# Kernel optimization log

Hardware: AMD Instinct MI355X
Metric: run time of the kernel (lower is better)

Reference implementation:

```python
import jax, jax.numpy as jnp
import numpy as np

EPS = 1e-12


def qsplit(x):
    # [..., 4n] with block layout [r|i|j|k] -> [..., n, 4]
    s = x.shape
    n = s[-1] // 4
    return jnp.swapaxes(x.reshape(s[:-1] + (4, n)), -1, -2)


def qmerge(q):
    # [..., n, 4] -> [..., 4n] block layout (transpose(-1,-2).view in torch)
    s = q.shape
    return jnp.swapaxes(q, -1, -2).reshape(s[:-2] + (s[-2] * 4,))


def qnormalize(q):
    # F.normalize(p=2, dim=-1)
    n = jnp.linalg.norm(q, axis=-1, keepdims=True)
    return q / jnp.maximum(n, EPS)


def qmul(q, r):
    # Hamilton product, last axis = (w, x, y, z)
    qw, qx, qy, qz = q[..., 0], q[..., 1], q[..., 2], q[..., 3]
    rw, rx, ry, rz = r[..., 0], r[..., 1], r[..., 2], r[..., 3]
    return jnp.stack([
        qw * rw - qx * rx - qy * ry - qz * rz,
        qw * rx + qx * rw + qy * rz - qz * ry,
        qw * ry - qx * rz + qy * rw + qz * rx,
        qw * rz + qx * ry - qy * rx + qz * rw,
    ], axis=-1)


def qlinear(x, W, b=None):
    # quaternion linear: x [..., 4*n_in], W [4, n_in, n_out]
    xr, xi, xj, xk = jnp.split(x, 4, axis=-1)
    Wr, Wi, Wj, Wk = W[0], W[1], W[2], W[3]
    out = jnp.concatenate([
        xr @ Wr - xi @ Wi - xj @ Wj - xk @ Wk,
        xr @ Wi + xi @ Wr + xj @ Wk - xk @ Wj,
        xr @ Wj - xi @ Wk + xj @ Wr + xk @ Wi,
        xr @ Wk + xi @ Wj - xj @ Wi + xk @ Wr,
    ], axis=-1)
    return out if b is None else out + b


def setup_inputs() -> dict:
    key = jax.random.key(0)
    ks = jax.random.split(key, 7)
    T_enc, T_tgt, B, D, H = 100, 26, 512, 96, 1024
    d4, h4 = D // 4, H // 4
    inp = jax.random.normal(ks[0], (T_enc, B, D), dtype=jnp.float32)
    target = jax.random.normal(ks[1], (T_tgt, B, D), dtype=jnp.float32)
    Wx = jax.random.normal(ks[2], (4, d4, h4), dtype=jnp.float32) * 0.05
    bx = jnp.zeros((H,), dtype=jnp.float32)
    Wh = jax.random.normal(ks[3], (4, h4, h4), dtype=jnp.float32) * 0.05
    Wl = jax.random.normal(ks[4], (4, h4, d4), dtype=jnp.float32) * 0.05
    bl = jnp.zeros((D,), dtype=jnp.float32)
    return {"inp": inp, "target": target, "Wx": Wx, "bx": bx, "Wh": Wh, "Wl": Wl, "bl": bl}


def reference(inp, target, Wx, bx, Wh, Wl, bl):
    B = inp.shape[1]
    H = Wh.shape[1] * 4

    def rnn_step(h, xt):
        h_new = jnp.tanh(qlinear(xt, Wx, bx) + qlinear(h, Wh))
        return h_new, h_new

    def predict(hseq, pre):
        # quaternion linear + per-quaternion L2 normalize + residual Hamilton product
        pred = qlinear(hseq, Wl, bl)
        qn = qnormalize(qsplit(pred))
        return qmerge(qmul(qn, qsplit(pre)))

    h0 = jnp.zeros((B, H), dtype=inp.dtype)
    h_last, hs = jax.lax.scan(rnn_step, h0, inp)  # hs: [T_enc, B, H]
    out_enc = predict(hs, inp)

    def dec_step(carry, _):
        h, x = carry
        h_new = jnp.tanh(qlinear(x, Wx, bx) + qlinear(h, Wh))
        pred = predict(h_new, x)
        return (h_new, pred), pred

    T_dec = target.shape[0] - 1
    _, out_dec = jax.lax.scan(dec_step, (h_last, target[0]), None, length=T_dec)
    return out_enc, out_dec
```

## Files before the change

### kernel.cpp

```cpp
#include <hip/hip_runtime.h>
#include <cstdint>

#define TENC 100
#define TDEC 25
#define BATCH 512
#define DIN 96
#define HDIM 1024

__device__ __constant__ int q_widx[4][4] = {{0,1,2,3},{1,0,3,2},{2,3,0,1},{3,2,1,0}};
__device__ __constant__ float q_sgn[4][4] = {{1.f,-1.f,-1.f,-1.f},
                                             {1.f, 1.f, 1.f,-1.f},
                                             {1.f,-1.f, 1.f, 1.f},
                                             {1.f, 1.f,-1.f, 1.f}};

__global__ void build_eff_kernel(const float* __restrict__ W, float* __restrict__ M,
                                 int nin, int nout) {
    int idx = blockIdx.x * blockDim.x + threadIdx.x;
    int ncol = nout * 4;
    int total = nin * 4 * ncol;
    if (idx >= total) return;
    int col = idx % ncol;
    int k = idx / ncol;
    int c = k / nin, m = k - c * nin;
    int comp = col / nout, o = col - comp * nout;
    M[idx] = q_sgn[comp][c] * W[(size_t)(q_widx[comp][c] * nin + m) * nout + o];
}

__device__ inline float xla_tanh(float x) {
    float ax = fabsf(x);
    if (ax < 0.0004f) return x;
    float t = fminf(fmaxf(x, -7.99881172180175781f), 7.99881172180175781f);
    float x2 = __fmul_rn(t, t);
    float p = -2.76076847742355e-16f;
    p = __fadd_rn(__fmul_rn(p, x2), 2.00018790482477e-13f);
    p = __fadd_rn(__fmul_rn(p, x2), -8.60467152213735e-11f);
    p = __fadd_rn(__fmul_rn(p, x2), 5.12229709037114e-08f);
    p = __fadd_rn(__fmul_rn(p, x2), 1.48572235717979e-05f);
    p = __fadd_rn(__fmul_rn(p, x2), 6.37261928875436e-04f);
    p = __fadd_rn(__fmul_rn(p, x2), 4.89352455891786e-03f);
    float num = __fmul_rn(t, p);
    float q = 1.19825839466702e-06f;
    q = __fadd_rn(__fmul_rn(q, x2), 1.18534705686654e-04f);
    q = __fadd_rn(__fmul_rn(q, x2), 2.26843463243900e-03f);
    q = __fadd_rn(__fmul_rn(q, x2), 4.89352518554385e-03f);
    return __fdiv_rn(num, q);
}

__global__ __launch_bounds__(256)
void rnn_part(const float* __restrict__ X,
              const float* __restrict__ Hin,
              const float* __restrict__ Mx,
              const float* __restrict__ Mh,
              float* __restrict__ parts) {
    __shared__ __align__(16) float As[2][64][68];
    __shared__ __align__(16) float Bs[2][64][64];
    __shared__ __align__(16) float Xs[24][68];
    __shared__ __align__(16) float Ms[24][64];

    const int tid = threadIdx.x;
    const int tx = tid & 15, ty = tid >> 4;
    const int c0 = blockIdx.x * 64;
    const int r0 = blockIdx.y * 64;
    const int z  = blockIdx.z;
    const int lk = tid & 63, lr = tid >> 6;
    const size_t SH = (size_t)BATCH * HDIM;

    float areg[16], breg[16];

    {
        const int k0 = z * 256;
        #pragma unroll
        for (int i = 0; i < 16; ++i)
            areg[i] = Hin[(size_t)(r0 + lr + 4 * i) * 1024 + k0 + lk];
        #pragma unroll
        for (int i = 0; i < 16; ++i)
            breg[i] = Mh[(size_t)(k0 + lr + 4 * i) * 1024 + c0 + lk];
    }
    #pragma unroll
    for (int i = 0; i < 6; ++i) {
        int idx = tid + 256 * i;
        int row = idx / 24, kk = idx - row * 24;
        Xs[kk][row] = X[(size_t)(r0 + row) * 96 + z * 24 + kk];
    }
    #pragma unroll
    for (int i = 0; i < 6; ++i) {
        int idx = tid + 256 * i;
        int kk = idx >> 6, col = idx & 63;
        Ms[kk][col] = Mx[(size_t)(z * 24 + kk) * 1024 + c0 + col];
    }
    #pragma unroll
    for (int i = 0; i < 16; ++i) As[0][lk][lr + 4 * i] = areg[i];
    #pragma unroll
    for (int i = 0; i < 16; ++i) Bs[0][lr + 4 * i][lk] = breg[i];
    __syncthreads();

    {
        float xa[4][4];
        #pragma unroll
        for (int i = 0; i < 4; ++i)
            #pragma unroll
            for (int j = 0; j < 4; ++j) xa[i][j] = 0.f;
        #pragma unroll 4
        for (int kk = 0; kk < 24; ++kk) {
            float4 av = *reinterpret_cast<const float4*>(&Xs[kk][ty * 4]);
            float4 bv = *reinterpret_cast<const float4*>(&Ms[kk][tx * 4]);
            float aa[4] = {av.x, av.y, av.z, av.w};
            float bb[4] = {bv.x, bv.y, bv.z, bv.w};
            #pragma unroll
            for (int i = 0; i < 4; ++i)
                #pragma unroll
                for (int j = 0; j < 4; ++j)
                    xa[i][j] = __fadd_rn(xa[i][j], __fmul_rn(aa[i], bb[j]));
        }
        float* pp = parts + (size_t)(4 + z) * SH;
        const int ccol = c0 + tx * 4;
        #pragma unroll
        for (int i = 0; i < 4; ++i)
            *reinterpret_cast<float4*>(pp + (size_t)(r0 + ty * 4 + i) * 1024 + ccol) =
                make_float4(xa[i][0], xa[i][1], xa[i][2], xa[i][3]);
    }

    float acc[4][4];
    #pragma unroll
    for (int i = 0; i < 4; ++i)
        #pragma unroll
        for (int j = 0; j < 4; ++j) acc[i][j] = 0.f;

    for (int kb = 0; kb < 4; ++kb) {
        const int cur = kb & 1;
        if (kb < 3) {
            const int k0 = z * 256 + (kb + 1) * 64;
            #pragma unroll
            for (int i = 0; i < 16; ++i)
                areg[i] = Hin[(size_t)(r0 + lr + 4 * i) * 1024 + k0 + lk];
            #pragma unroll
            for (int i = 0; i < 16; ++i)
                breg[i] = Mh[(size_t)(k0 + lr + 4 * i) * 1024 + c0 + lk];
        }
        #pragma unroll 8
        for (int k = 0; k < 64; ++k) {
            float4 av = *reinterpret_cast<const float4*>(&As[cur][k][ty * 4]);
            float4 bv = *reinterpret_cast<const float4*>(&Bs[cur][k][tx * 4]);
            float aa[4] = {av.x, av.y, av.z, av.w};
            float bb[4] = {bv.x, bv.y, bv.z, bv.w};
            #pragma unroll
            for (int i = 0; i < 4; ++i)
                #pragma unroll
                for (int j = 0; j < 4; ++j)
                    acc[i][j] = __fadd_rn(acc[i][j], __fmul_rn(aa[i], bb[j]));
        }
        if (kb < 3) {
            #pragma unroll
            for (int i = 0; i < 16; ++i) As[cur ^ 1][lk][lr + 4 * i] = areg[i];
            #pragma unroll
            for (int i = 0; i < 16; ++i) Bs[cur ^ 1][lr + 4 * i][lk] = breg[i];
            __syncthreads();
        }
    }

    float* pp = parts + (size_t)z * SH;
    const int ccol = c0 + tx * 4;
    #pragma unroll
    for (int i = 0; i < 4; ++i)
        *reinterpret_cast<float4*>(pp + (size_t)(r0 + ty * 4 + i) * 1024 + ccol) =
            make_float4(acc[i][0], acc[i][1], acc[i][2], acc[i][3]);
}

__global__ __launch_bounds__(256)
void rnn_combine(const float* __restrict__ parts, const float* __restrict__ bx,
                 float* __restrict__ Hout) {
    int t = blockIdx.x * blockDim.x + threadIdx.x;
    int i = t * 4;
    int col = i & 1023;
    const size_t SH = (size_t)BATCH * HDIM;
    float4 h0 = *reinterpret_cast<const float4*>(parts + 0 * SH + i);
    float4 h1 = *reinterpret_cast<const float4*>(parts + 1 * SH + i);
    float4 h2 = *reinterpret_cast<const float4*>(parts + 2 * SH + i);
    float4 h3 = *reinterpret_cast<const float4*>(parts + 3 * SH + i);
    float4 x0 = *reinterpret_cast<const float4*>(parts + 4 * SH + i);
    float4 x1 = *reinterpret_cast<const float4*>(parts + 5 * SH + i);
    float4 x2 = *reinterpret_cast<const float4*>(parts + 6 * SH + i);
    float4 x3 = *reinterpret_cast<const float4*>(parts + 7 * SH + i);
    float4 bb = *reinterpret_cast<const float4*>(bx + col);
    float h0v[4] = {h0.x, h0.y, h0.z, h0.w};
    float h1v[4] = {h1.x, h1.y, h1.z, h1.w};
    float h2v[4] = {h2.x, h2.y, h2.z, h2.w};
    float h3v[4] = {h3.x, h3.y, h3.z, h3.w};
    float x0v[4] = {x0.x, x0.y, x0.z, x0.w};
    float x1v[4] = {x1.x, x1.y, x1.z, x1.w};
    float x2v[4] = {x2.x, x2.y, x2.z, x2.w};
    float x3v[4] = {x3.x, x3.y, x3.z, x3.w};
    float bv[4]  = {bb.x, bb.y, bb.z, bb.w};
    float o[4];
    #pragma unroll
    for (int j = 0; j < 4; ++j) {
        float xcb = __fadd_rn(__fadd_rn(__fadd_rn(x0v[j], x1v[j]), x2v[j]), x3v[j]);
        float hcb = __fadd_rn(__fadd_rn(__fadd_rn(h0v[j], h1v[j]), h2v[j]), h3v[j]);
        float rs  = __fadd_rn(__fadd_rn(xcb, bv[j]), hcb);
        o[j] = xla_tanh(rs);
    }
    *reinterpret_cast<float4*>(Hout + i) = make_float4(o[0], o[1], o[2], o[3]);
}

__global__ __launch_bounds__(256)
void predict_qmul(const float* __restrict__ H,
                  const float* __restrict__ Ml,
                  const float* __restrict__ bl,
                  const float* __restrict__ pre,
                  float* __restrict__ out) {
    __shared__ float lds[10752];
    float* As = lds;
    float* Bs = lds + 4352;
    float* Ps = lds;

    const int tid = threadIdx.x;
    const int tx = tid & 15, ty = tid >> 4;
    const int r0 = blockIdx.x * 64;
    const int lk = tid & 63, lr = tid >> 6;

    float hcb[4][6], ha[4][6];
    #pragma unroll
    for (int i = 0; i < 4; ++i)
        #pragma unroll
        for (int j = 0; j < 6; ++j) { hcb[i][j] = 0.f; ha[i][j] = 0.f; }

    for (int kb = 0; kb < 16; ++kb) {
        __syncthreads();
        #pragma unroll
        for (int i = 0; i < 16; ++i)
            As[lk * 68 + lr + 4 * i] = H[(size_t)(r0 + lr + 4 * i) * 1024 + kb * 64 + lk];
        #pragma unroll
        for (int i = 0; i < 24; ++i) {
            int idx = tid + 256 * i;
            int k = idx / 96, c = idx - k * 96;
            Bs[k * 100 + c] = Ml[(size_t)(kb * 64 + k) * 96 + c];
        }
        __syncthreads();
        #pragma unroll 4
        for (int k = 0; k < 64; ++k) {
            float4 av = *reinterpret_cast<const float4*>(&As[k * 68 + ty * 4]);
            const float* bp = &Bs[k * 100 + tx * 6];
            float2 b0 = *reinterpret_cast<const float2*>(bp);
            float2 b1 = *reinterpret_cast<const float2*>(bp + 2);
            float2 b2 = *reinterpret_cast<const float2*>(bp + 4);
            float aa[4] = {av.x, av.y, av.z, av.w};
            float bb[6] = {b0.x, b0.y, b1.x, b1.y, b2.x, b2.y};
            #pragma unroll
            for (int i = 0; i < 4; ++i)
                #pragma unroll
                for (int j = 0; j < 6; ++j)
                    ha[i][j] = __fadd_rn(ha[i][j], __fmul_rn(aa[i], bb[j]));
        }
        if ((kb & 3) == 3) {
            #pragma unroll
            for (int i = 0; i < 4; ++i)
                #pragma unroll
                for (int j = 0; j < 6; ++j) {
                    hcb[i][j] = __fadd_rn(hcb[i][j], ha[i][j]);
                    ha[i][j] = 0.f;
                }
        }
    }

    __syncthreads();
    #pragma unroll
    for (int i = 0; i < 4; ++i)
        #pragma unroll
        for (int j = 0; j < 6; ++j) {
            int c = tx * 6 + j;
            Ps[(ty * 4 + i) * 100 + c] = __fadd_rn(hcb[i][j], bl[c]);
        }
    __syncthreads();

    #pragma unroll
    for (int i = 0; i < 6; ++i) {
        int q = tid + 256 * i;
        int row = q / 24, n = q - row * 24;
        const float* p = &Ps[row * 100 + n];
        float pw = p[0], px = p[24], py = p[48], pz = p[72];
        float s = __fadd_rn(__fadd_rn(__fadd_rn(__fmul_rn(pw, pw), __fmul_rn(px, px)),
                                      __fmul_rn(py, py)), __fmul_rn(pz, pz));
        float nr = sqrtf(s);
        float nm = fmaxf(nr, 1e-12f);
        pw = __fdiv_rn(pw, nm); px = __fdiv_rn(px, nm);
        py = __fdiv_rn(py, nm); pz = __fdiv_rn(pz, nm);
        const float* r = pre + (size_t)(r0 + row) * 96 + n;
        float rw = r[0], rx = r[24], ry = r[48], rz = r[72];
        float* o = out + (size_t)(r0 + row) * 96 + n;
        o[0]  = __fsub_rn(__fsub_rn(__fsub_rn(__fmul_rn(pw, rw), __fmul_rn(px, rx)),
                                    __fmul_rn(py, ry)), __fmul_rn(pz, rz));
        o[24] = __fsub_rn(__fadd_rn(__fadd_rn(__fmul_rn(pw, rx), __fmul_rn(px, rw)),
                                    __fmul_rn(py, rz)), __fmul_rn(pz, ry));
        o[48] = __fadd_rn(__fadd_rn(__fsub_rn(__fmul_rn(pw, ry), __fmul_rn(px, rz)),
                                    __fmul_rn(py, rw)), __fmul_rn(pz, rx));
        o[72] = __fadd_rn(__fsub_rn(__fadd_rn(__fmul_rn(pw, rz), __fmul_rn(px, ry)),
                                    __fmul_rn(py, rx)), __fmul_rn(pz, rw));
    }
}

__global__ __launch_bounds__(256)
void predict_part(const float* __restrict__ H,
                  const float* __restrict__ Ml,
                  float* __restrict__ ppart) {
    __shared__ float As[64][18];
    __shared__ float Bs[64][100];

    const int tid = threadIdx.x;
    const int tx = tid & 15, ty = tid >> 4;
    const int r0 = blockIdx.x * 16;
    const int z  = blockIdx.y;

    float acc[6];
    #pragma unroll
    for (int j = 0; j < 6; ++j) acc[j] = 0.f;

    for (int kb = 0; kb < 4; ++kb) {
        const int k0 = z * 256 + kb * 64;
        __syncthreads();
        #pragma unroll
        for (int i = 0; i < 4; ++i) {
            int idx = tid + 256 * i;
            int k = idx & 63, row = idx >> 6;
            As[k][row] = H[(size_t)(r0 + row) * 1024 + k0 + k];
        }
        #pragma unroll
        for (int i = 0; i < 24; ++i) {
            int idx = tid + 256 * i;
            int k = idx / 96, c = idx - k * 96;
            Bs[k][c] = Ml[(size_t)(k0 + k) * 96 + c];
        }
        __syncthreads();
        #pragma unroll 8
        for (int k = 0; k < 64; ++k) {
            float a = As[k][ty];
            const float* bp = &Bs[k][tx * 6];
            float2 b0 = *reinterpret_cast<const float2*>(bp);
            float2 b1 = *reinterpret_cast<const float2*>(bp + 2);
            float2 b2 = *reinterpret_cast<const float2*>(bp + 4);
            float bb[6] = {b0.x, b0.y, b1.x, b1.y, b2.x, b2.y};
            #pragma unroll
            for (int j = 0; j < 6; ++j)
                acc[j] = __fadd_rn(acc[j], __fmul_rn(a, bb[j]));
        }
    }

    float* pp = ppart + (size_t)z * (BATCH * DIN);
    #pragma unroll
    for (int j = 0; j < 6; ++j)
        pp[(size_t)(r0 + ty) * 96 + tx * 6 + j] = acc[j];
}

__global__ void combine_qmul(const float* __restrict__ ppart,
                             const float* __restrict__ bl,
                             const float* __restrict__ pre,
                             float* __restrict__ out, int M) {
    int q = blockIdx.x * blockDim.x + threadIdx.x;
    if (q >= M * 24) return;
    int b = q / 24, n = q - b * 24;
    const size_t SP = (size_t)BATCH * DIN;
    float pq[4];
    #pragma unroll
    for (int comp = 0; comp < 4; ++comp) {
        size_t idx = (size_t)b * 96 + comp * 24 + n;
        float p0 = ppart[0 * SP + idx];
        float p1 = ppart[1 * SP + idx];
        float p2 = ppart[2 * SP + idx];
        float p3 = ppart[3 * SP + idx];
        pq[comp] = __fadd_rn(__fadd_rn(__fadd_rn(__fadd_rn(p0, p1), p2), p3),
                             bl[comp * 24 + n]);
    }
    float pw = pq[0], px = pq[1], py = pq[2], pz = pq[3];
    float s = __fadd_rn(__fadd_rn(__fadd_rn(__fmul_rn(pw, pw), __fmul_rn(px, px)),
                                  __fmul_rn(py, py)), __fmul_rn(pz, pz));
    float nr = sqrtf(s);
    float nm = fmaxf(nr, 1e-12f);
    pw = __fdiv_rn(pw, nm); px = __fdiv_rn(px, nm);
    py = __fdiv_rn(py, nm); pz = __fdiv_rn(pz, nm);
    const float* r = pre + (size_t)b * 96 + n;
    float rw = r[0], rx = r[24], ry = r[48], rz = r[72];
    float* o = out + (size_t)b * 96 + n;
    o[0]  = __fsub_rn(__fsub_rn(__fsub_rn(__fmul_rn(pw, rw), __fmul_rn(px, rx)),
                                __fmul_rn(py, ry)), __fmul_rn(pz, rz));
    o[24] = __fsub_rn(__fadd_rn(__fadd_rn(__fmul_rn(pw, rx), __fmul_rn(px, rw)),
                                __fmul_rn(py, rz)), __fmul_rn(pz, ry));
    o[48] = __fadd_rn(__fadd_rn(__fsub_rn(__fmul_rn(pw, ry), __fmul_rn(px, rz)),
                                __fmul_rn(py, rw)), __fmul_rn(pz, rx));
    o[72] = __fadd_rn(__fsub_rn(__fadd_rn(__fmul_rn(pw, rz), __fmul_rn(px, ry)),
                                __fmul_rn(py, rx)), __fmul_rn(pz, rw));
}

extern "C" void kernel_launch(void* const* d_in, const int* in_sizes, int n_in,
                              void* d_out, int out_size, void* d_ws, size_t ws_size,
                              hipStream_t stream) {
    const float* inp    = (const float*)d_in[0];
    const float* target = (const float*)d_in[1];
    const float* Wx     = (const float*)d_in[2];
    const float* bx     = (const float*)d_in[3];
    const float* Wh     = (const float*)d_in[4];
    const float* Wl     = (const float*)d_in[5];
    const float* bl     = (const float*)d_in[6];

    float* out = (float*)d_out;
    float* out_enc = out;
    float* out_dec = out + (size_t)TENC * BATCH * DIN;

    const size_t SH = (size_t)BATCH * HDIM;
    const size_t SX = (size_t)BATCH * DIN;

    size_t off = 0;
    auto alloc = [&](size_t nf) -> float* {
        float* p = (float*)((char*)d_ws + off);
        off += nf * sizeof(float);
        return p;
    };
    float* M_x   = alloc((size_t)DIN * HDIM);
    float* M_h   = alloc((size_t)HDIM * HDIM);
    float* M_l   = alloc((size_t)HDIM * DIN);
    float* hs    = alloc((size_t)(TENC + 1) * SH);
    float* parts = alloc(8 * SH);
    float* ppart = alloc(4 * SX);

    {
        int t1 = 4 * 24 * 4 * 256;
        build_eff_kernel<<<(t1 + 255) / 256, 256, 0, stream>>>(Wx, M_x, 24, 256);
        int t2 = 4 * 256 * 4 * 256;
        build_eff_kernel<<<(t2 + 255) / 256, 256, 0, stream>>>(Wh, M_h, 256, 256);
        int t3 = 4 * 256 * 4 * 24;
        build_eff_kernel<<<(t3 + 255) / 256, 256, 0, stream>>>(Wl, M_l, 256, 24);
    }

    hipMemsetAsync(hs, 0, SH * sizeof(float), stream);

    dim3 gPart(HDIM / 64, BATCH / 64, 4);
    const int gComb = (int)(SH / 4 / 256);

    for (int t = 0; t < TENC; ++t) {
        rnn_part<<<gPart, 256, 0, stream>>>(
            inp + (size_t)t * SX, hs + (size_t)t * SH, M_x, M_h, parts);
        rnn_combine<<<gComb, 256, 0, stream>>>(parts, bx, hs + (size_t)(t + 1) * SH);
    }
    predict_qmul<<<(TENC * BATCH) / 64, 256, 0, stream>>>(
        hs + SH, M_l, bl, inp, out_enc);

    const float* x = target;
    float* hin = hs + (size_t)TENC * SH;
    dim3 gPPart(BATCH / 16, 4);
    for (int t = 0; t < TDEC; ++t) {
        float* hout = (t & 1) ? (hs + SH) : hs;
        rnn_part<<<gPart, 256, 0, stream>>>(x, hin, M_x, M_h, parts);
        rnn_combine<<<gComb, 256, 0, stream>>>(parts, bx, hout);
        predict_part<<<gPPart, 256, 0, stream>>>(hout, M_l, ppart);
        int nq = BATCH * 24;
        combine_qmul<<<(nq + 255) / 256, 256, 0, stream>>>(
            ppart, bl, x, out_dec + (size_t)t * SX, BATCH);
        x = out_dec + (size_t)t * SX;
        hin = hout;
    }
}
```

Measured before the change: 3.980 ms.

## Restructure recurrent GEMM to stage only weights in LDS and read H uniformly

Replaces the 64x64 register-tiled GEMM, which staged both the hidden-state and weight tiles in shared memory, with a 512-thread kernel in which each wavefront owns 8 batch rows and each lane owns one output column. Only the weight tiles go through LDS, with float4 loads. Hidden-state and input values are read directly from global memory at wave-uniform addresses, which the compiler can turn into scalar loads. This removes the transposed LDS stores for the A tile, but each weight value loaded from LDS now feeds only 8 FMAs instead of 16 per 8 loads, and the A reads depend on scalar loads and the cache.

```diff
diff --git a/kernel.cpp b/kernel.cpp
--- a/kernel.cpp
+++ b/kernel.cpp
@@ -46,124 +46,92 @@
     return __fdiv_rn(num, q);
 }
 
-__global__ __launch_bounds__(256)
-void rnn_part(const float* __restrict__ X,
-              const float* __restrict__ Hin,
-              const float* __restrict__ Mx,
-              const float* __restrict__ Mh,
-              float* __restrict__ parts) {
-    __shared__ __align__(16) float As[2][64][68];
+__global__ __launch_bounds__(512)
+void rnn_part_sm(const float* __restrict__ X,
+                 const float* __restrict__ Hin,
+                 const float* __restrict__ Mx,
+                 const float* __restrict__ Mh,
+                 float* __restrict__ parts) {
     __shared__ __align__(16) float Bs[2][64][64];
-    __shared__ __align__(16) float Xs[24][68];
-    __shared__ __align__(16) float Ms[24][64];
-
-    const int tid = threadIdx.x;
-    const int tx = tid & 15, ty = tid >> 4;
+    __shared__ __align__(16) float Bsx[24][64];
+
+    const int tid  = threadIdx.x;
+    const int lane = tid & 63;
+    const int wid  = __builtin_amdgcn_readfirstlane(tid >> 6);
     const int c0 = blockIdx.x * 64;
-    const int r0 = blockIdx.y * 64;
+    const int r0 = blockIdx.y * 64 + wid * 8;
     const int z  = blockIdx.z;
-    const int lk = tid & 63, lr = tid >> 6;
     const size_t SH = (size_t)BATCH * HDIM;
-
-    float areg[16], breg[16];
+    const int cc = c0 + lane;
+
+    for (int i = tid; i < 24 * 64; i += 512) {
+        int kk = i >> 6, c = i & 63;
+        Bsx[kk][c] = Mx[(size_t)(z * 24 + kk) * 1024 + c0 + c];
+    }
+    #pragma unroll
+    for (int i = 0; i < 2; ++i) {
+        int idx = tid + 512 * i;
+        int kk = idx >> 4, cg = (idx & 15) * 4;
+        *reinterpret_cast<float4*>(&Bs[0][kk][cg]) =
+            *reinterpret_cast<const float4*>(&Mh[(size_t)(z * 256 + kk) * 1024 + c0 + cg]);
+    }
+    __syncthreads();
 
     {
-        const int k0 = z * 256;
-        #pragma unroll
-        for (int i = 0; i < 16; ++i)
-            areg[i] = Hin[(size_t)(r0 + lr + 4 * i) * 1024 + k0 + lk];
-        #pragma unroll
-        for (int i = 0; i < 16; ++i)
-            breg[i] = Mh[(size_t)(k0 + lr + 4 * i) * 1024 + c0 + lk];
-    }
-    #pragma unroll
-    for (int i = 0; i < 6; ++i) {
-        int idx = tid + 256 * i;
-        int row = idx / 24, kk = idx - row * 24;
-        Xs[kk][row] = X[(size_t)(r0 + row) * 96 + z * 24 + kk];
-    }
-    #pragma unroll
-    for (int i = 0; i < 6; ++i) {
-        int idx = tid + 256 * i;
-        int kk = idx >> 6, col = idx & 63;
-        Ms[kk][col] = Mx[(size_t)(z * 24 + kk) * 1024 + c0 + col];
-    }
-    #pragma unroll
-    for (int i = 0; i < 16; ++i) As[0][lk][lr + 4 * i] = areg[i];
-    #pragma unroll
-    for (int i = 0; i < 16; ++i) Bs[0][lr + 4 * i][lk] = breg[i];
-    __syncthreads();
-
-    {
-        float xa[4][4];
-        #pragma unroll
-        for (int i = 0; i < 4; ++i)
+        float xacc[8];
+        #pragma unroll
+        for (int j = 0; j < 8; ++j) xacc[j] = 0.f;
+        #pragma unroll
+        for (int k = 0; k < 24; ++k) {
+            float w = Bsx[k][lane];
             #pragma unroll
-            for (int j = 0; j < 4; ++j) xa[i][j] = 0.f;
-        #pragma unroll 4
-        for (int kk = 0; kk < 24; ++kk) {
-            float4 av = *reinterpret_cast<const float4*>(&Xs[kk][ty * 4]);
-            float4 bv = *reinterpret_cast<const float4*>(&Ms[kk][tx * 4]);
-            float aa[4] = {av.x, av.y, av.z, av.w};
-            float bb[4] = {bv.x, bv.y, bv.z, bv.w};
-            #pragma unroll
-            for (int i = 0; i < 4; ++i)
-                #pragma unroll
-                for (int j = 0; j < 4; ++j)
-                    xa[i][j] = __fadd_rn(xa[i][j], __fmul_rn(aa[i], bb[j]));
+            for (int j = 0; j < 8; ++j) {
+                float a = X[(size_t)(r0 + j) * 96 + z * 24 + k];
+                xacc[j] = __fadd_rn(xacc[j], __fmul_rn(a, w));
+            }
         }
         float* pp = parts + (size_t)(4 + z) * SH;
-        const int ccol = c0 + tx * 4;
-        #pragma unroll
-        for (int i = 0; i < 4; ++i)
-            *reinterpret_cast<float4*>(pp + (size_t)(r0 + ty * 4 + i) * 1024 + ccol) =
-                make_float4(xa[i][0], xa[i][1], xa[i][2], xa[i][3]);
-    }
-
-    float acc[4][4];
-    #pragma unroll
-    for (int i = 0; i < 4; ++i)
-        #pragma unroll
-        for (int j = 0; j < 4; ++j) acc[i][j] = 0.f;
-
+        #pragma unroll
+        for (int j = 0; j < 8; ++j)
+            pp[(size_t)(r0 + j) * 1024 + cc] = xacc[j];
+    }
+
+    float acc[8];
+    #pragma unroll
+    for (int j = 0; j < 8; ++j) acc[j] = 0.f;
+
+    #pragma unroll
     for (int kb = 0; kb < 4; ++kb) {
         const int cur = kb & 1;
+        float4 nb0, nb1;
         if (kb < 3) {
-            const int k0 = z * 256 + (kb + 1) * 64;
+            int idx0 = tid, idx1 = tid + 512;
+            nb0 = *reinterpret_cast<const float4*>(
+                &Mh[(size_t)(z * 256 + (kb + 1) * 64 + (idx0 >> 4)) * 1024 + c0 + (idx0 & 15) * 4]);
+            nb1 = *reinterpret_cast<const float4*>(
+                &Mh[(size_t)(z * 256 + (kb + 1) * 64 + (idx1 >> 4)) * 1024 + c0 + (idx1 & 15) * 4]);
+        }
+        #pragma unroll 16
+        for (int k = 0; k < 64; ++k) {
+            float w = Bs[cur][k][lane];
             #pragma unroll
-            for (int i = 0; i < 16; ++i)
-                areg[i] = Hin[(size_t)(r0 + lr + 4 * i) * 1024 + k0 + lk];
-            #pragma unroll
-            for (int i = 0; i < 16; ++i)
-                breg[i] = Mh[(size_t)(k0 + lr + 4 * i) * 1024 + c0 + lk];
-        }
-        #pragma unroll 8
-        for (int k = 0; k < 64; ++k) {
-            float4 av = *reinterpret_cast<const float4*>(&As[cur][k][ty * 4]);
-            float4 bv = *reinterpret_cast<const float4*>(&Bs[cur][k][tx * 4]);
-            float aa[4] = {av.x, av.y, av.z, av.w};
-            float bb[4] = {bv.x, bv.y, bv.z, bv.w};
-            #pragma unroll
-            for (int i = 0; i < 4; ++i)
-                #pragma unroll
-                for (int j = 0; j < 4; ++j)
-                    acc[i][j] = __fadd_rn(acc[i][j], __fmul_rn(aa[i], bb[j]));
+            for (int j = 0; j < 8; ++j) {
+                float a = Hin[(size_t)(r0 + j) * 1024 + z * 256 + kb * 64 + k];
+                acc[j] = __fadd_rn(acc[j], __fmul_rn(a, w));
+            }
         }
         if (kb < 3) {
-            #pragma unroll
-            for (int i = 0; i < 16; ++i) As[cur ^ 1][lk][lr + 4 * i] = areg[i];
-            #pragma unroll
-            for (int i = 0; i < 16; ++i) Bs[cur ^ 1][lr + 4 * i][lk] = breg[i];
+            int idx0 = tid, idx1 = tid + 512;
+            *reinterpret_cast<float4*>(&Bs[cur ^ 1][idx0 >> 4][(idx0 & 15) * 4]) = nb0;
+            *reinterpret_cast<float4*>(&Bs[cur ^ 1][idx1 >> 4][(idx1 & 15) * 4]) = nb1;
             __syncthreads();
         }
     }
 
     float* pp = parts + (size_t)z * SH;
-    const int ccol = c0 + tx * 4;
-    #pragma unroll
-    for (int i = 0; i < 4; ++i)
-        *reinterpret_cast<float4*>(pp + (size_t)(r0 + ty * 4 + i) * 1024 + ccol) =
-            make_float4(acc[i][0], acc[i][1], acc[i][2], acc[i][3]);
+    #pragma unroll
+    for (int j = 0; j < 8; ++j)
+        pp[(size_t)(r0 + j) * 1024 + cc] = acc[j];
 }
 
 __global__ __launch_bounds__(256)
@@ -435,7 +403,7 @@
     const int gComb = (int)(SH / 4 / 256);
 
     for (int t = 0; t < TENC; ++t) {
-        rnn_part<<<gPart, 256, 0, stream>>>(
+        rnn_part_sm<<<gPart, 512, 0, stream>>>(
             inp + (size_t)t * SX, hs + (size_t)t * SH, M_x, M_h, parts);
         rnn_combine<<<gComb, 256, 0, stream>>>(parts, bx, hs + (size_t)(t + 1) * SH);
     }
@@ -447,7 +415,7 @@
     dim3 gPPart(BATCH / 16, 4);
     for (int t = 0; t < TDEC; ++t) {
         float* hout = (t & 1) ? (hs + SH) : hs;
-        rnn_part<<<gPart, 256, 0, stream>>>(x, hin, M_x, M_h, parts);
+        rnn_part_sm<<<gPart, 512, 0, stream>>>(x, hin, M_x, M_h, parts);
         rnn_combine<<<gComb, 256, 0, stream>>>(parts, bx, hout);
         predict_part<<<gPPart, 256, 0, stream>>>(hout, M_l, ppart);
         int nq = BATCH * 24;
```

Measured after the change: 6.209 ms. 56.0% more time.
